# Optimization experiments

Hardware: AMD Instinct MI355X
Metric: run time of the kernel (lower is better)

Reference implementation:

```python
import jax, jax.numpy as jnp
import numpy as np
from jax import lax


def _fps(xyz, num_group):
    """Farthest point sampling. xyz: (B, N, 3) -> centers (B, G, 3).
    Sequential over G (structural loop) via lax.scan; starts at index 0."""
    B, N, _ = xyz.shape

    def step(carry, _):
        min_d, last_idx = carry                      # (B, N), (B,)
        last_pt = jax.vmap(lambda p, i: p[i])(xyz, last_idx)  # (B, 3)
        d = jnp.sum((xyz - last_pt[:, None, :]) ** 2, axis=-1)  # (B, N)
        min_d = jnp.minimum(min_d, d)
        nxt = jnp.argmax(min_d, axis=-1).astype(jnp.int32)
        return (min_d, nxt), last_idx

    init = (jnp.full((B, N), jnp.inf, dtype=xyz.dtype),
            jnp.zeros((B,), dtype=jnp.int32))
    _, idxs = lax.scan(step, init, None, length=num_group)  # (G, B)
    idxs = idxs.T                                            # (B, G)
    centers = jax.vmap(lambda p, i: p[i])(xyz, idxs)         # (B, G, 3)
    return centers


def setup_inputs() -> dict:
    key = jax.random.key(0)
    xyz = jax.random.normal(key, (32, 8192, 3), dtype=jnp.float32)
    return {"xyz": xyz, "num_group": 256, "group_size": 32}


def reference(xyz, num_group, group_size):
    B, N, C = xyz.shape
    center = _fps(xyz, num_group)                            # (B, G, 3)
    # dense pairwise distances: (B, G, N)
    dist = jnp.linalg.norm(center[:, :, None, :] - xyz[:, None, :, :], axis=-1)
    _, idx = lax.top_k(-dist, group_size)                    # (B, G, k) smallest dists
    # gather neighbors per batch: (B, G, k, 3)
    patch = jax.vmap(lambda pts, i: pts[i])(xyz, idx)
    patch = patch - center[:, :, None, :]                    # recenter
    return (patch, center)
```

## Files before the change

kernel.cpp:

```cpp
#include <hip/hip_runtime.h>

#pragma clang fp contract(off)

#define BB 32
#define NN 8192
#define GG 256
#define KK 32

#define TFPS 512
#define JPF (NN / TFPS)

template <int CTRL>
__device__ __forceinline__ float rot_maxf(float v) {
  const int o =
      __builtin_amdgcn_update_dpp(0, __float_as_int(v), CTRL, 0xF, 0xF, true);
  return fmaxf(v, __int_as_float(o));
}

__global__ __launch_bounds__(TFPS, 1) void fps_kernel(const float* __restrict__ xyz,
                                                      float* __restrict__ out) {
#pragma clang fp contract(off)
  const int b = blockIdx.x;
  const int t = threadIdx.x;
  const int lane = t & 63;
  const int wave = t >> 6;
  const float* __restrict__ P = xyz + (size_t)b * NN * 3;

  __shared__ float4 pts[NN];
  __shared__ float rowmax[2][32];
  __shared__ unsigned winIdx[2];

  float px[JPF], py[JPF], pz[JPF], md[JPF];
#pragma unroll
  for (int j = 0; j < JPF; ++j) {
    const int idx = t + j * TFPS;
    const float x = P[idx * 3 + 0];
    const float y = P[idx * 3 + 1];
    const float z = P[idx * 3 + 2];
    px[j] = x; py[j] = y; pz[j] = z;
    md[j] = __builtin_inff();
    pts[idx] = make_float4(x, y, z, 0.0f);
  }
  if (t == 0) { winIdx[0] = 0xFFFFFFFFu; winIdx[1] = 0xFFFFFFFFu; }
  __syncthreads();

  unsigned win = 0;
  unsigned mywin = 0;

  for (int i = 0; i < GG; ++i) {
    if (t == i) mywin = win;
    if (i == GG - 1) break;

    const float4 c = pts[win];
    const float cx = c.x, cy = c.y, cz = c.z;

    float bv = -1.0f;
#pragma unroll
    for (int j = 0; j < JPF; ++j) {
      const float dx = px[j] - cx;
      const float dy = py[j] - cy;
      const float dz = pz[j] - cz;
      const float d = dx * dx + dy * dy + dz * dz;
      const float m = md[j] < d ? md[j] : d;
      md[j] = m;
      bv = fmaxf(bv, m);
    }

    float r = bv;
    r = rot_maxf<0x121>(r);
    r = rot_maxf<0x122>(r);
    r = rot_maxf<0x124>(r);
    r = rot_maxf<0x128>(r);
    if ((lane & 15) == 0)
      rowmax[i & 1][wave * 4 + (lane >> 4)] = r;
    __syncthreads();

    if (t == 0) winIdx[(i + 1) & 1] = 0xFFFFFFFFu;

    const float* __restrict__ rm = rowmax[i & 1];
    const int g = lane & 15;
    float m2 = fmaxf(rm[g], rm[g + 16]);
    m2 = rot_maxf<0x121>(m2);
    m2 = rot_maxf<0x122>(m2);
    m2 = rot_maxf<0x124>(m2);
    m2 = rot_maxf<0x128>(m2);
    const float M = m2;

    if (bv == M) {
      int fj = 0;
#pragma unroll
      for (int j = JPF - 1; j >= 0; --j)
        if (md[j] == M) fj = j;
      atomicMin(&winIdx[i & 1], (unsigned)t + ((unsigned)fj << 9));
    }
    __syncthreads();

    win = winIdx[i & 1];
  }

  if (t < GG) {
    const float4 c = pts[mywin];
    float* __restrict__ co =
        out + (size_t)BB * GG * KK * 3 + ((size_t)b * GG + t) * 3;
    co[0] = c.x; co[1] = c.y; co[2] = c.z;
  }
}

__global__ __launch_bounds__(512, 1) void knn_kernel(const float* __restrict__ xyz,
                                                     float* __restrict__ out) {
#pragma clang fp contract(off)
  const int b = blockIdx.x >> 3;
  const int chunk = blockIdx.x & 7;
  const int t = threadIdx.x;
  const int lane = t & 63;
  const int wave = t >> 6;
  const float* __restrict__ P = xyz + (size_t)b * NN * 3;

  __shared__ float xs[NN], ys[NN], zs[NN];
  __shared__ unsigned long long cand[8][256];

  for (int pt = t; pt < NN; pt += 512) {
    xs[pt] = P[pt * 3 + 0];
    ys[pt] = P[pt * 3 + 1];
    zs[pt] = P[pt * 3 + 2];
  }
  __syncthreads();

  const float* __restrict__ cent = out + (size_t)BB * GG * KK * 3;

  for (int gi = 0; gi < 4; ++gi) {
    const int g = chunk * 32 + wave * 4 + gi;
    const float cx = cent[((size_t)b * GG + g) * 3 + 0];
    const float cy = cent[((size_t)b * GG + g) * 3 + 1];
    const float cz = cent[((size_t)b * GG + g) * 3 + 2];

    float d2r[128];
    float mn = __builtin_inff();
#pragma unroll
    for (int j = 0; j < 128; ++j) {
      const int idx = lane + j * 64;
      const float dx = xs[idx] - cx;
      const float dy = ys[idx] - cy;
      const float dz = zs[idx] - cz;
      const float d2 = dx * dx + dy * dy + dz * dz;
      d2r[j] = d2;
      mn = fminf(mn, d2);
    }

    float sm = mn;
#pragma unroll
    for (int k = 2; k <= 64; k <<= 1) {
#pragma unroll
      for (int j2 = k >> 1; j2 > 0; j2 >>= 1) {
        const float o = __shfl_xor(sm, j2, 64);
        const bool keepMin = (((lane & k) == 0) == ((lane & j2) == 0));
        sm = keepMin ? fminf(sm, o) : fmaxf(sm, o);
      }
    }
    const float v = __shfl(sm, 31, 64);
    const float vi = __uint_as_float(__float_as_uint(v) + 8);

    unsigned cnt = 0;
    unsigned long long* __restrict__ cb = cand[wave];
#pragma unroll
    for (int j = 0; j < 128; ++j) {
      const bool p = d2r[j] <= vi;
      const unsigned long long mk = __ballot(p);
      if (p) {
        const unsigned off = cnt + (unsigned)__popcll(mk & ((1ull << lane) - 1));
        if (off < 256)
          cb[off] = ((unsigned long long)__float_as_uint(d2r[j]) << 32) |
                    (unsigned)(lane + j * 64);
      }
      cnt += (unsigned)__popcll(mk);
    }
    if (cnt > 256) cnt = 256;

    auto conv = [](unsigned long long e) -> unsigned long long {
      const float d = sqrtf(__uint_as_float((unsigned)(e >> 32)));
      return ((unsigned long long)__float_as_uint(d) << 32) | (e & 0xFFFFFFFFull);
    };

    unsigned long long myk;
    if (cnt <= 64) {
      unsigned long long key = ~0ull;
      if ((unsigned)lane < cnt) key = conv(cb[lane]);
#pragma unroll
      for (int k = 2; k <= 64; k <<= 1) {
#pragma unroll
        for (int j2 = k >> 1; j2 > 0; j2 >>= 1) {
          const unsigned long long o = __shfl_xor(key, j2, 64);
          const bool keepMin = (((lane & k) == 0) == ((lane & j2) == 0));
          const unsigned long long lo = o < key ? o : key;
          const unsigned long long hi = o < key ? key : o;
          key = keepMin ? lo : hi;
        }
      }
      myk = key;
    } else {
      unsigned long long k0 = ~0ull, k1 = ~0ull, k2 = ~0ull, k3 = ~0ull;
      if ((unsigned)lane < cnt)         k0 = conv(cb[lane]);
      if ((unsigned)(lane + 64) < cnt)  k1 = conv(cb[lane + 64]);
      if ((unsigned)(lane + 128) < cnt) k2 = conv(cb[lane + 128]);
      if ((unsigned)(lane + 192) < cnt) k3 = conv(cb[lane + 192]);
      unsigned long long got = ~0ull;
      for (int r = 0; r < 32; ++r) {
        unsigned long long m01 = k0 < k1 ? k0 : k1;
        unsigned long long m23 = k2 < k3 ? k2 : k3;
        unsigned long long m = m01 < m23 ? m01 : m23;
#pragma unroll
        for (int s = 32; s > 0; s >>= 1) {
          const unsigned long long o = __shfl_xor(m, s, 64);
          m = o < m ? o : m;
        }
        if (lane == r) got = m;
        if (k0 == m) k0 = ~0ull;
        else if (k1 == m) k1 = ~0ull;
        else if (k2 == m) k2 = ~0ull;
        else if (k3 == m) k3 = ~0ull;
      }
      myk = got;
    }

    if (lane < KK) {
      const unsigned idx = (unsigned)(myk & 0xFFFFFFFFull);
      const float ox = xs[idx] - cx;
      const float oy = ys[idx] - cy;
      const float oz = zs[idx] - cz;
      float* __restrict__ po = out + ((size_t)(((size_t)b * GG + g) * KK + lane)) * 3;
      po[0] = ox; po[1] = oy; po[2] = oz;
    }
  }
}

extern "C" void kernel_launch(void* const* d_in, const int* in_sizes, int n_in,
                              void* d_out, int out_size, void* d_ws, size_t ws_size,
                              hipStream_t stream) {
  const float* xyz = (const float*)d_in[0];
  float* out = (float*)d_out;
  fps_kernel<<<dim3(BB), dim3(TFPS), 0, stream>>>(xyz, out);
  knn_kernel<<<dim3(BB * 8), dim3(512), 0, stream>>>(xyz, out);
}
```

Measured before the change: 339.1 us.

## Fuse FPS argmax into packed value-index DPP reduction with single barrier

Each FPS iteration now reduces a packed (distance, inverted index) key across the wave with DPP row shifts and row_bcast steps, then does one 64-bit shared atomicMax per wave into a three-slot rotating buffer. This replaces the two-phase scheme that needed two barriers per iteration, a shared rowmax table, a second reduction and an atomicMin. Halving the barriers on the serial 255-step loop is the goal. The cost is twice as many DPP operations with 64-bit compares, and the result depends on the row_bcast controls behaving correctly on this target.

```diff
diff --git a/kernel.cpp b/kernel.cpp
--- a/kernel.cpp
+++ b/kernel.cpp
@@ -11,10 +11,14 @@
 #define JPF (NN / TFPS)
 
 template <int CTRL>
-__device__ __forceinline__ float rot_maxf(float v) {
-  const int o =
-      __builtin_amdgcn_update_dpp(0, __float_as_int(v), CTRL, 0xF, 0xF, true);
-  return fmaxf(v, __int_as_float(o));
+__device__ __forceinline__ void dpp_max(unsigned& hi, unsigned& lo) {
+  const unsigned ohi =
+      (unsigned)__builtin_amdgcn_update_dpp(0, (int)hi, CTRL, 0xF, 0xF, true);
+  const unsigned olo =
+      (unsigned)__builtin_amdgcn_update_dpp(0, (int)lo, CTRL, 0xF, 0xF, true);
+  const bool gt = (ohi > hi) || ((ohi == hi) && (olo > lo));
+  hi = gt ? ohi : hi;
+  lo = gt ? olo : lo;
 }
 
 __global__ __launch_bounds__(TFPS, 1) void fps_kernel(const float* __restrict__ xyz,
@@ -23,12 +27,10 @@
   const int b = blockIdx.x;
   const int t = threadIdx.x;
   const int lane = t & 63;
-  const int wave = t >> 6;
   const float* __restrict__ P = xyz + (size_t)b * NN * 3;
 
   __shared__ float4 pts[NN];
-  __shared__ float rowmax[2][32];
-  __shared__ unsigned winIdx[2];
+  __shared__ unsigned long long slot[3];
 
   float px[JPF], py[JPF], pz[JPF], md[JPF];
 #pragma unroll
@@ -41,7 +43,7 @@
     md[j] = __builtin_inff();
     pts[idx] = make_float4(x, y, z, 0.0f);
   }
-  if (t == 0) { winIdx[0] = 0xFFFFFFFFu; winIdx[1] = 0xFFFFFFFFu; }
+  if (t == 0) { slot[0] = 0; slot[1] = 0; slot[2] = 0; }
   __syncthreads();
 
   unsigned win = 0;
@@ -55,6 +57,7 @@
     const float cx = c.x, cy = c.y, cz = c.z;
 
     float bv = -1.0f;
+    int bj = 0;
 #pragma unroll
     for (int j = 0; j < JPF; ++j) {
       const float dx = px[j] - cx;
@@ -63,39 +66,26 @@
       const float d = dx * dx + dy * dy + dz * dz;
       const float m = md[j] < d ? md[j] : d;
       md[j] = m;
-      bv = fmaxf(bv, m);
-    }
-
-    float r = bv;
-    r = rot_maxf<0x121>(r);
-    r = rot_maxf<0x122>(r);
-    r = rot_maxf<0x124>(r);
-    r = rot_maxf<0x128>(r);
-    if ((lane & 15) == 0)
-      rowmax[i & 1][wave * 4 + (lane >> 4)] = r;
+      if (m > bv) { bv = m; bj = j; }
+    }
+    const unsigned bi = (unsigned)t + ((unsigned)bj << 9);
+
+    unsigned hi = __float_as_uint(bv);
+    unsigned lo = ~bi;
+    dpp_max<0x121>(hi, lo);
+    dpp_max<0x122>(hi, lo);
+    dpp_max<0x124>(hi, lo);
+    dpp_max<0x128>(hi, lo);
+    dpp_max<0x142>(hi, lo);
+    dpp_max<0x143>(hi, lo);
+
+    if (lane == 63)
+      atomicMax(&slot[i % 3], ((unsigned long long)hi << 32) | lo);
+    if (t == 0) slot[(i + 1) % 3] = 0;
     __syncthreads();
 
-    if (t == 0) winIdx[(i + 1) & 1] = 0xFFFFFFFFu;
-
-    const float* __restrict__ rm = rowmax[i & 1];
-    const int g = lane & 15;
-    float m2 = fmaxf(rm[g], rm[g + 16]);
-    m2 = rot_maxf<0x121>(m2);
-    m2 = rot_maxf<0x122>(m2);
-    m2 = rot_maxf<0x124>(m2);
-    m2 = rot_maxf<0x128>(m2);
-    const float M = m2;
-
-    if (bv == M) {
-      int fj = 0;
-#pragma unroll
-      for (int j = JPF - 1; j >= 0; --j)
-        if (md[j] == M) fj = j;
-      atomicMin(&winIdx[i & 1], (unsigned)t + ((unsigned)fj << 9));
-    }
-    __syncthreads();
-
-    win = winIdx[i & 1];
+    const unsigned long long k = slot[i % 3];
+    win = ~(unsigned)k;
   }
 
   if (t < GG) {
```

New measurement: 351.0 us. 3.5% more time.

## Use per-wave packed max/index reduction to drop second barrier in FPS

Applied to the files above, without the earlier changes.

The FPS argmax step now finds each wave's max and its lowest winning index with DPP row_bcast reductions and a readlane. Each wave writes one packed 64-bit key (distance bits high, inverted index low) to shared memory. After a single barrier every thread scans the 8 keys itself, which removes the shared atomicMin and the second __syncthreads per iteration. This adds a second DPP reduction chain and a serial 8-entry scan in every thread, and ties across waves rely on the inverted index encoding to pick the lowest index.

```diff
diff --git a/kernel.cpp b/kernel.cpp
--- a/kernel.cpp
+++ b/kernel.cpp
@@ -11,10 +11,17 @@
 #define JPF (NN / TFPS)
 
 template <int CTRL>
-__device__ __forceinline__ float rot_maxf(float v) {
+__device__ __forceinline__ float dppmax_f(float v) {
   const int o =
       __builtin_amdgcn_update_dpp(0, __float_as_int(v), CTRL, 0xF, 0xF, true);
   return fmaxf(v, __int_as_float(o));
+}
+
+template <int CTRL>
+__device__ __forceinline__ unsigned dppmax_u(unsigned v) {
+  const unsigned o =
+      (unsigned)__builtin_amdgcn_update_dpp(0, (int)v, CTRL, 0xF, 0xF, true);
+  return o > v ? o : v;
 }
 
 __global__ __launch_bounds__(TFPS, 1) void fps_kernel(const float* __restrict__ xyz,
@@ -27,8 +34,7 @@
   const float* __restrict__ P = xyz + (size_t)b * NN * 3;
 
   __shared__ float4 pts[NN];
-  __shared__ float rowmax[2][32];
-  __shared__ unsigned winIdx[2];
+  __shared__ unsigned long long warr[2][8];
 
   float px[JPF], py[JPF], pz[JPF], md[JPF];
 #pragma unroll
@@ -41,7 +47,6 @@
     md[j] = __builtin_inff();
     pts[idx] = make_float4(x, y, z, 0.0f);
   }
-  if (t == 0) { winIdx[0] = 0xFFFFFFFFu; winIdx[1] = 0xFFFFFFFFu; }
   __syncthreads();
 
   unsigned win = 0;
@@ -66,36 +71,43 @@
       bv = fmaxf(bv, m);
     }
 
-    float r = bv;
-    r = rot_maxf<0x121>(r);
-    r = rot_maxf<0x122>(r);
-    r = rot_maxf<0x124>(r);
-    r = rot_maxf<0x128>(r);
-    if ((lane & 15) == 0)
-      rowmax[i & 1][wave * 4 + (lane >> 4)] = r;
+    float v = bv;
+    v = dppmax_f<0x121>(v);
+    v = dppmax_f<0x122>(v);
+    v = dppmax_f<0x124>(v);
+    v = dppmax_f<0x128>(v);
+    v = dppmax_f<0x142>(v);
+    v = dppmax_f<0x143>(v);
+    const unsigned Mw =
+        (unsigned)__builtin_amdgcn_readlane(__float_as_int(v), 63);
+
+    unsigned cbi = 0u;
+    if (__float_as_uint(bv) == Mw) {
+      int fj = 0;
+#pragma unroll
+      for (int j = JPF - 1; j >= 0; --j)
+        if (__float_as_uint(md[j]) == Mw) fj = j;
+      cbi = ~((unsigned)t + ((unsigned)fj << 9));
+    }
+    cbi = dppmax_u<0x121>(cbi);
+    cbi = dppmax_u<0x122>(cbi);
+    cbi = dppmax_u<0x124>(cbi);
+    cbi = dppmax_u<0x128>(cbi);
+    cbi = dppmax_u<0x142>(cbi);
+    cbi = dppmax_u<0x143>(cbi);
+
+    if (lane == 63)
+      warr[i & 1][wave] = ((unsigned long long)Mw << 32) | cbi;
     __syncthreads();
 
-    if (t == 0) winIdx[(i + 1) & 1] = 0xFFFFFFFFu;
-
-    const float* __restrict__ rm = rowmax[i & 1];
-    const int g = lane & 15;
-    float m2 = fmaxf(rm[g], rm[g + 16]);
-    m2 = rot_maxf<0x121>(m2);
-    m2 = rot_maxf<0x122>(m2);
-    m2 = rot_maxf<0x124>(m2);
-    m2 = rot_maxf<0x128>(m2);
-    const float M = m2;
-
-    if (bv == M) {
-      int fj = 0;
-#pragma unroll
-      for (int j = JPF - 1; j >= 0; --j)
-        if (md[j] == M) fj = j;
-      atomicMin(&winIdx[i & 1], (unsigned)t + ((unsigned)fj << 9));
-    }
-    __syncthreads();
-
-    win = winIdx[i & 1];
+    const unsigned long long* __restrict__ w = warr[i & 1];
+    unsigned long long best = w[0];
+#pragma unroll
+    for (int k = 1; k < 8; ++k) {
+      const unsigned long long e = w[k];
+      best = e > best ? e : best;
+    }
+    win = ~(unsigned)best;
   }
 
   if (t < GG) {
```

New measurement: 343.3 us. Within noise of the previous version (+1.3%).

## Double FPS threads to 1024 and recompute KNN distances instead of caching

Applied to the files above, without the earlier changes.

The FPS kernel now runs 1024 threads per block, so each thread holds 8 points. The per-wave max reduction uses DPP row broadcasts down to one value per wave, and the cross-wave max is read as four float4 loads instead of a second DPP pass. The KNN kernel stops keeping 128 distances per lane in registers and recomputes them from LDS in the ballot pass, with partial unrolling, to cut register pressure. The cost is more block-level sync overhead across 16 waves in FPS and the extra distance arithmetic and LDS reads in KNN.

```diff
diff --git a/kernel.cpp b/kernel.cpp
--- a/kernel.cpp
+++ b/kernel.cpp
@@ -7,11 +7,11 @@
 #define GG 256
 #define KK 32
 
-#define TFPS 512
+#define TFPS 1024
 #define JPF (NN / TFPS)
 
 template <int CTRL>
-__device__ __forceinline__ float rot_maxf(float v) {
+__device__ __forceinline__ float dppmax_f(float v) {
   const int o =
       __builtin_amdgcn_update_dpp(0, __float_as_int(v), CTRL, 0xF, 0xF, true);
   return fmaxf(v, __int_as_float(o));
@@ -27,7 +27,7 @@
   const float* __restrict__ P = xyz + (size_t)b * NN * 3;
 
   __shared__ float4 pts[NN];
-  __shared__ float rowmax[2][32];
+  __shared__ float wmax[2][16];
   __shared__ unsigned winIdx[2];
 
   float px[JPF], py[JPF], pz[JPF], md[JPF];
@@ -66,32 +66,33 @@
       bv = fmaxf(bv, m);
     }
 
-    float r = bv;
-    r = rot_maxf<0x121>(r);
-    r = rot_maxf<0x122>(r);
-    r = rot_maxf<0x124>(r);
-    r = rot_maxf<0x128>(r);
-    if ((lane & 15) == 0)
-      rowmax[i & 1][wave * 4 + (lane >> 4)] = r;
+    float v = bv;
+    v = dppmax_f<0x121>(v);
+    v = dppmax_f<0x122>(v);
+    v = dppmax_f<0x124>(v);
+    v = dppmax_f<0x128>(v);
+    v = dppmax_f<0x142>(v);
+    v = dppmax_f<0x143>(v);
+    if (lane == 63) wmax[i & 1][wave] = v;
     __syncthreads();
 
     if (t == 0) winIdx[(i + 1) & 1] = 0xFFFFFFFFu;
 
-    const float* __restrict__ rm = rowmax[i & 1];
-    const int g = lane & 15;
-    float m2 = fmaxf(rm[g], rm[g + 16]);
-    m2 = rot_maxf<0x121>(m2);
-    m2 = rot_maxf<0x122>(m2);
-    m2 = rot_maxf<0x124>(m2);
-    m2 = rot_maxf<0x128>(m2);
-    const float M = m2;
-
-    if (bv == M) {
+    const float4* __restrict__ rm4 = (const float4*)wmax[i & 1];
+    const float4 a0 = rm4[0], a1 = rm4[1], a2 = rm4[2], a3 = rm4[3];
+    const float m0 = fmaxf(fmaxf(a0.x, a0.y), fmaxf(a0.z, a0.w));
+    const float m1 = fmaxf(fmaxf(a1.x, a1.y), fmaxf(a1.z, a1.w));
+    const float m2 = fmaxf(fmaxf(a2.x, a2.y), fmaxf(a2.z, a2.w));
+    const float m3 = fmaxf(fmaxf(a3.x, a3.y), fmaxf(a3.z, a3.w));
+    const float M = fmaxf(fmaxf(m0, m1), fmaxf(m2, m3));
+    const unsigned Mu = __float_as_uint(M);
+
+    if (__float_as_uint(bv) == Mu) {
       int fj = 0;
 #pragma unroll
       for (int j = JPF - 1; j >= 0; --j)
-        if (md[j] == M) fj = j;
-      atomicMin(&winIdx[i & 1], (unsigned)t + ((unsigned)fj << 9));
+        if (__float_as_uint(md[j]) == Mu) fj = j;
+      atomicMin(&winIdx[i & 1], (unsigned)t + ((unsigned)fj << 10));
     }
     __syncthreads();
 
@@ -134,16 +135,14 @@
     const float cy = cent[((size_t)b * GG + g) * 3 + 1];
     const float cz = cent[((size_t)b * GG + g) * 3 + 2];
 
-    float d2r[128];
     float mn = __builtin_inff();
-#pragma unroll
+#pragma unroll 8
     for (int j = 0; j < 128; ++j) {
       const int idx = lane + j * 64;
       const float dx = xs[idx] - cx;
       const float dy = ys[idx] - cy;
       const float dz = zs[idx] - cz;
       const float d2 = dx * dx + dy * dy + dz * dz;
-      d2r[j] = d2;
       mn = fminf(mn, d2);
     }
 
@@ -162,15 +161,20 @@
 
     unsigned cnt = 0;
     unsigned long long* __restrict__ cb = cand[wave];
-#pragma unroll
+#pragma unroll 8
     for (int j = 0; j < 128; ++j) {
-      const bool p = d2r[j] <= vi;
+      const int idx = lane + j * 64;
+      const float dx = xs[idx] - cx;
+      const float dy = ys[idx] - cy;
+      const float dz = zs[idx] - cz;
+      const float d2 = dx * dx + dy * dy + dz * dz;
+      const bool p = d2 <= vi;
       const unsigned long long mk = __ballot(p);
       if (p) {
         const unsigned off = cnt + (unsigned)__popcll(mk & ((1ull << lane) - 1));
         if (off < 256)
-          cb[off] = ((unsigned long long)__float_as_uint(d2r[j]) << 32) |
-                    (unsigned)(lane + j * 64);
+          cb[off] = ((unsigned long long)__float_as_uint(d2) << 32) |
+                    (unsigned)idx;
       }
       cnt += (unsigned)__popcll(mk);
     }
```

Result: slower. 358.6 us (+5.8%).
